# Performance work log

Measured on AMD Instinct MI355X. Metric: run time of the kernel, lower is better.

The kernel has to match this reference:

```python
import jax, jax.numpy as jnp
import numpy as np

NUM_NODES = 50000
NUM_EDGES = 800000
DIM = 96


def setup_inputs() -> dict:
    key = jax.random.key(0)
    k1, k2, k3, k4, k5, k6 = jax.random.split(key, 6)
    x = jax.random.normal(k1, (NUM_NODES, DIM), dtype=jnp.float32)
    edge_index = jax.random.randint(k2, (2, NUM_EDGES), 0, NUM_NODES, dtype=jnp.int64)
    s = 1.0 / np.sqrt(DIM)
    W_self = jax.random.uniform(k3, (DIM, DIM), dtype=jnp.float32, minval=-s, maxval=s)
    b_self = jax.random.uniform(k4, (DIM,), dtype=jnp.float32, minval=-s, maxval=s)
    W_neigh = jax.random.uniform(k5, (DIM, DIM), dtype=jnp.float32, minval=-s, maxval=s)
    b_neigh = jax.random.uniform(k6, (DIM,), dtype=jnp.float32, minval=-s, maxval=s)
    return {"x": x, "edge_index": edge_index, "W_self": W_self, "b_self": b_self,
            "W_neigh": W_neigh, "b_neigh": b_neigh}


def reference(x, edge_index, W_self, b_self, W_neigh, b_neigh):
    source, target = edge_index[0], edge_index[1]
    # scatter-add of gathered source features into target rows
    aggregated = jax.ops.segment_sum(x[source], target, num_segments=NUM_NODES)  # [N, D]
    degree = jax.ops.segment_sum(jnp.ones((NUM_EDGES,), dtype=x.dtype), target,
                                 num_segments=NUM_NODES)[:, None]  # [N, 1]
    neighbor_mean = aggregated / jnp.maximum(degree, 1.0)
    # nn.Linear applies x @ W.T + b
    return x @ W_self.T + b_self + neighbor_mean @ W_neigh.T + b_neigh
```

## Files before the change

### kernel.cpp

```cpp
#include <hip/hip_runtime.h>
#include <hip/hip_bf16.h>

#define N_NODES 50000
#define N_EDGES 800000
#define DIM 96
#define NPART 256
#define PSZ 196
#define NBINBLK 196
#define BINCAP 48
#define BPP (NBINBLK * BINCAP)
#define CAP 4096
#define NPACK_BLOCKS 4688

typedef unsigned int uint;
typedef unsigned short u16;

__device__ __forceinline__ u16 f2bf(float f) {
    __hip_bfloat16 h = __float2bfloat16(f);
    return *reinterpret_cast<u16*>(&h);
}
__device__ __forceinline__ float bf2f(u16 u) {
    return __uint_as_float(((uint)u) << 16);
}
__device__ __forceinline__ int pdiv(int t) { return (int)(((uint)t * 85599u) >> 24); }

__global__ __launch_bounds__(256) void packbin_k(
    const float* __restrict__ x, const int* __restrict__ ei,
    u16* __restrict__ xbf, uint* __restrict__ part_edges,
    int* __restrict__ counts)
{
    __shared__ uint bins[NPART * BINCAP];
    __shared__ int  bcnt[NPART];
    const int tid = threadIdx.x;

    if (blockIdx.x >= NBINBLK) {
        int pb = blockIdx.x - NBINBLK;
        int i4 = (pb * 256 + tid) * 4;
        if (i4 < N_NODES * DIM) {
            float4 v = *reinterpret_cast<const float4*>(x + i4);
            ushort4 o;
            o.x = f2bf(v.x); o.y = f2bf(v.y); o.z = f2bf(v.z); o.w = f2bf(v.w);
            *reinterpret_cast<ushort4*>(xbf + i4) = o;
        }
        return;
    }

    for (int i = tid; i < NPART; i += 256) bcnt[i] = 0;
    __syncthreads();

    const int e0 = blockIdx.x * 4096 + tid * 16;
    if (e0 + 16 <= N_EDGES) {
#pragma unroll
        for (int j = 0; j < 4; j++) {
            int4 s = *reinterpret_cast<const int4*>(ei + e0 + j * 4);
            int4 t = *reinterpret_cast<const int4*>(ei + N_EDGES + e0 + j * 4);
            int ss[4] = {s.x, s.y, s.z, s.w};
            int tt[4] = {t.x, t.y, t.z, t.w};
#pragma unroll
            for (int k = 0; k < 4; k++) {
                int p = pdiv(tt[k]);
                int local = tt[k] - p * PSZ;
                int slot = atomicAdd(&bcnt[p], 1);
                if (slot < BINCAP)
                    bins[p * BINCAP + slot] = ((uint)local << 16) | (uint)ss[k];
            }
        }
    } else {
        for (int j = 0; j < 16; j++) {
            int e = e0 + j;
            if (e < N_EDGES) {
                int sv = ei[e];
                int tv = ei[N_EDGES + e];
                int p = pdiv(tv);
                int local = tv - p * PSZ;
                int slot = atomicAdd(&bcnt[p], 1);
                if (slot < BINCAP)
                    bins[p * BINCAP + slot] = ((uint)local << 16) | (uint)sv;
            }
        }
    }
    __syncthreads();

    for (int p = tid; p < NPART; p += 256)
        counts[p * NBINBLK + blockIdx.x] = min(bcnt[p], BINCAP);

    for (int i = tid; i < NPART * BINCAP; i += 256) {
        int p = i / BINCAP;
        int s = i - p * BINCAP;
        if (s < bcnt[p])
            part_edges[(size_t)p * BPP + blockIdx.x * BINCAP + s] = bins[i];
    }
}

__global__ __launch_bounds__(1024) void fused_k(
    const u16* __restrict__ xbf,
    const uint* __restrict__ part_edges,
    const int* __restrict__ counts,
    const float* __restrict__ Wself, const float* __restrict__ bself,
    const float* __restrict__ Wneigh, const float* __restrict__ bneigh,
    float* __restrict__ out)
{
    using short8 = __attribute__((ext_vector_type(8))) short;
    using f32x4  = __attribute__((ext_vector_type(4))) float;

    __shared__ u16   Axm[208 * 200];
    __shared__ short Bb[96 * 200];
    __shared__ uint  recs[CAP];
    __shared__ u16   ssrc[CAP];
    __shared__ int   bc[256];
    __shared__ int   csc[256];
    __shared__ int   hist[256];
    __shared__ int   cur[256];

    const int tid = threadIdx.x;
    const int p = blockIdx.x;
    const int node0 = p * PSZ;

    for (int idx = tid; idx < 96 * 96; idx += 1024) {
        int j = idx / 96;
        int k = idx - j * 96;
        Bb[j * 200 + k]      = (short)f2bf(Wself[idx]);
        Bb[j * 200 + 96 + k] = (short)f2bf(Wneigh[idx]);
    }

    if (tid < 256) {
        int v = (tid < NBINBLK) ? counts[p * NBINBLK + tid] : 0;
        bc[tid] = v;
        csc[tid] = v;
        cur[tid] = 0;
    }

    for (int i = tid; i < PSZ * 12; i += 1024) {
        int n = i / 12, t = i - n * 12;
        int node = node0 + n;
        short8 v = (short8)0;
        if (node < N_NODES)
            v = *reinterpret_cast<const short8*>(xbf + (size_t)node * DIM + t * 8);
        *reinterpret_cast<short8*>(&Axm[n * 200 + t * 8]) = v;
    }
    __syncthreads();

    for (int o = 1; o < 256; o <<= 1) {
        int v = 0;
        if (tid < 256 && tid >= o) v = csc[tid - o];
        __syncthreads();
        if (tid < 256) csc[tid] += v;
        __syncthreads();
    }
    int m = csc[255]; if (m > CAP) m = CAP;

    for (int i = tid; i < NBINBLK * BINCAP; i += 1024) {
        int b = i / BINCAP;
        int s = i - b * BINCAP;
        if (s < bc[b]) {
            int dst = csc[b] - bc[b] + s;
            if (dst < CAP)
                recs[dst] = part_edges[(size_t)p * BPP + i];
        }
    }
    __syncthreads();

    for (int i = tid; i < m; i += 1024)
        atomicAdd(&cur[recs[i] >> 16], 1);
    __syncthreads();
    if (tid < 256) hist[tid] = cur[tid];
    __syncthreads();
    for (int o = 1; o < 256; o <<= 1) {
        int v = 0;
        if (tid < 256 && tid >= o) v = hist[tid - o];
        __syncthreads();
        if (tid < 256) hist[tid] += v;
        __syncthreads();
    }
    if (tid < 256) cur[tid] = hist[tid] - cur[tid];
    __syncthreads();

    for (int i = tid; i < m; i += 1024) {
        uint r = recs[i];
        int pos = atomicAdd(&cur[r >> 16], 1);
        ssrc[pos] = (u16)(r & 0xFFFF);
    }
    __syncthreads();

    if (tid < 1008) {
        const int g = tid / 24;
        const int l = tid - g * 24;
        const int l4 = l * 4;
        for (int r = g; r < PSZ; r += 42) {
            int end = hist[r];
            int beg = (r > 0) ? hist[r - 1] : 0;
            float ax = 0.f, ay = 0.f, az = 0.f, aw = 0.f;
            int i = beg;
            for (; i + 3 < end; i += 4) {
                int s0 = ssrc[i], s1 = ssrc[i + 1], s2 = ssrc[i + 2], s3 = ssrc[i + 3];
                ushort4 v0 = *reinterpret_cast<const ushort4*>(xbf + (size_t)s0 * DIM + l4);
                ushort4 v1 = *reinterpret_cast<const ushort4*>(xbf + (size_t)s1 * DIM + l4);
                ushort4 v2 = *reinterpret_cast<const ushort4*>(xbf + (size_t)s2 * DIM + l4);
                ushort4 v3 = *reinterpret_cast<const ushort4*>(xbf + (size_t)s3 * DIM + l4);
                ax += bf2f(v0.x) + bf2f(v1.x) + bf2f(v2.x) + bf2f(v3.x);
                ay += bf2f(v0.y) + bf2f(v1.y) + bf2f(v2.y) + bf2f(v3.y);
                az += bf2f(v0.z) + bf2f(v1.z) + bf2f(v2.z) + bf2f(v3.z);
                aw += bf2f(v0.w) + bf2f(v1.w) + bf2f(v2.w) + bf2f(v3.w);
            }
            for (; i < end; i++) {
                int s = ssrc[i];
                ushort4 v = *reinterpret_cast<const ushort4*>(xbf + (size_t)s * DIM + l4);
                ax += bf2f(v.x); ay += bf2f(v.y); az += bf2f(v.z); aw += bf2f(v.w);
            }
            float inv = (end > beg) ? 1.0f / (float)(end - beg) : 0.f;
            ushort4 o;
            o.x = f2bf(ax * inv); o.y = f2bf(ay * inv);
            o.z = f2bf(az * inv); o.w = f2bf(aw * inv);
            *reinterpret_cast<ushort4*>(&Axm[r * 200 + 96 + l4]) = o;
        }
    }
    __syncthreads();

    const int wave = tid >> 6;
    const int lane = tid & 63;
    const int quad = lane >> 4;
    const int m16  = lane & 15;

    if (wave < 13) {
        const int rloc = wave * 16;
        f32x4 acc[6];
#pragma unroll
        for (int nt = 0; nt < 6; nt++) acc[nt] = (f32x4){0.f, 0.f, 0.f, 0.f};

#pragma unroll
        for (int kt = 0; kt < 6; kt++) {
            short8 a = *reinterpret_cast<const short8*>(
                &Axm[(rloc + m16) * 200 + kt * 32 + quad * 8]);
#pragma unroll
            for (int nt = 0; nt < 6; nt++) {
                short8 b = *reinterpret_cast<const short8*>(
                    &Bb[(nt * 16 + m16) * 200 + kt * 32 + quad * 8]);
                acc[nt] = __builtin_amdgcn_mfma_f32_16x16x32_bf16(a, b, acc[nt], 0, 0, 0);
            }
        }

#pragma unroll
        for (int nt = 0; nt < 6; nt++) {
            int col = nt * 16 + m16;
            float bias = bself[col] + bneigh[col];
#pragma unroll
            for (int reg = 0; reg < 4; reg++) {
                int rl = rloc + quad * 4 + reg;
                int row = node0 + rl;
                if (rl < PSZ && row < N_NODES)
                    out[(size_t)row * DIM + col] = acc[nt][reg] + bias;
            }
        }
    }
}

extern "C" void kernel_launch(void* const* d_in, const int* in_sizes, int n_in,
                              void* d_out, int out_size, void* d_ws, size_t ws_size,
                              hipStream_t stream) {
    const float* x      = (const float*)d_in[0];
    const int*   ei     = (const int*)d_in[1];
    const float* Wself  = (const float*)d_in[2];
    const float* bself  = (const float*)d_in[3];
    const float* Wneigh = (const float*)d_in[4];
    const float* bneigh = (const float*)d_in[5];
    float* out = (float*)d_out;

    uint* part_edges = (uint*)d_ws;
    int*  counts     = (int*)(part_edges + (size_t)NPART * BPP);
    u16*  xbf        = (u16*)(counts + NPART * NBINBLK);

    packbin_k<<<NBINBLK + NPACK_BLOCKS, 256, 0, stream>>>(
        x, ei, xbf, part_edges, counts);
    fused_k<<<NPART, 1024, 0, stream>>>(
        xbf, part_edges, counts, Wself, bself, Wneigh, bneigh, out);
}
```

Baseline: 126.8 us.

## Merge binning and fused compute into one cooperative kernel with grid sync

Replaces the two-kernel pipeline (bin/pack kernel then fused aggregate+GEMM kernel) with a single cooperative launch of 256 blocks of 1024 threads. Each block first converts part of x to bf16 and bins its slice of edges into shared memory, then a grid-wide sync separates this from the per-partition aggregation and MFMA phase. It removes one kernel launch boundary and lets the W staging overlap the binning, at the cost of fewer, larger binning blocks (lower parallelism in phase one), grid sync overhead, and a single large shared-memory buffer reused across phases.

```diff
diff --git a/kernel.cpp b/kernel.cpp
--- a/kernel.cpp
+++ b/kernel.cpp
@@ -1,16 +1,18 @@
 #include <hip/hip_runtime.h>
 #include <hip/hip_bf16.h>
+#include <hip/hip_cooperative_groups.h>
 
 #define N_NODES 50000
 #define N_EDGES 800000
 #define DIM 96
 #define NPART 256
 #define PSZ 196
-#define NBINBLK 196
 #define BINCAP 48
-#define BPP (NBINBLK * BINCAP)
+#define BPP (NPART * BINCAP)
 #define CAP 4096
-#define NPACK_BLOCKS 4688
+#define EPB (N_EDGES / NPART)
+
+namespace cg = cooperative_groups;
 
 typedef unsigned int uint;
 typedef unsigned short u16;
@@ -24,97 +26,30 @@
 }
 __device__ __forceinline__ int pdiv(int t) { return (int)(((uint)t * 85599u) >> 24); }
 
-__global__ __launch_bounds__(256) void packbin_k(
+__global__ __launch_bounds__(1024) void sage_all_k(
     const float* __restrict__ x, const int* __restrict__ ei,
-    u16* __restrict__ xbf, uint* __restrict__ part_edges,
-    int* __restrict__ counts)
-{
-    __shared__ uint bins[NPART * BINCAP];
-    __shared__ int  bcnt[NPART];
-    const int tid = threadIdx.x;
-
-    if (blockIdx.x >= NBINBLK) {
-        int pb = blockIdx.x - NBINBLK;
-        int i4 = (pb * 256 + tid) * 4;
-        if (i4 < N_NODES * DIM) {
-            float4 v = *reinterpret_cast<const float4*>(x + i4);
-            ushort4 o;
-            o.x = f2bf(v.x); o.y = f2bf(v.y); o.z = f2bf(v.z); o.w = f2bf(v.w);
-            *reinterpret_cast<ushort4*>(xbf + i4) = o;
-        }
-        return;
-    }
-
-    for (int i = tid; i < NPART; i += 256) bcnt[i] = 0;
-    __syncthreads();
-
-    const int e0 = blockIdx.x * 4096 + tid * 16;
-    if (e0 + 16 <= N_EDGES) {
-#pragma unroll
-        for (int j = 0; j < 4; j++) {
-            int4 s = *reinterpret_cast<const int4*>(ei + e0 + j * 4);
-            int4 t = *reinterpret_cast<const int4*>(ei + N_EDGES + e0 + j * 4);
-            int ss[4] = {s.x, s.y, s.z, s.w};
-            int tt[4] = {t.x, t.y, t.z, t.w};
-#pragma unroll
-            for (int k = 0; k < 4; k++) {
-                int p = pdiv(tt[k]);
-                int local = tt[k] - p * PSZ;
-                int slot = atomicAdd(&bcnt[p], 1);
-                if (slot < BINCAP)
-                    bins[p * BINCAP + slot] = ((uint)local << 16) | (uint)ss[k];
-            }
-        }
-    } else {
-        for (int j = 0; j < 16; j++) {
-            int e = e0 + j;
-            if (e < N_EDGES) {
-                int sv = ei[e];
-                int tv = ei[N_EDGES + e];
-                int p = pdiv(tv);
-                int local = tv - p * PSZ;
-                int slot = atomicAdd(&bcnt[p], 1);
-                if (slot < BINCAP)
-                    bins[p * BINCAP + slot] = ((uint)local << 16) | (uint)sv;
-            }
-        }
-    }
-    __syncthreads();
-
-    for (int p = tid; p < NPART; p += 256)
-        counts[p * NBINBLK + blockIdx.x] = min(bcnt[p], BINCAP);
-
-    for (int i = tid; i < NPART * BINCAP; i += 256) {
-        int p = i / BINCAP;
-        int s = i - p * BINCAP;
-        if (s < bcnt[p])
-            part_edges[(size_t)p * BPP + blockIdx.x * BINCAP + s] = bins[i];
-    }
-}
-
-__global__ __launch_bounds__(1024) void fused_k(
-    const u16* __restrict__ xbf,
-    const uint* __restrict__ part_edges,
-    const int* __restrict__ counts,
     const float* __restrict__ Wself, const float* __restrict__ bself,
     const float* __restrict__ Wneigh, const float* __restrict__ bneigh,
-    float* __restrict__ out)
+    u16* __restrict__ xbf, uint* __restrict__ part_edges,
+    int* __restrict__ counts, float* __restrict__ out)
 {
     using short8 = __attribute__((ext_vector_type(8))) short;
     using f32x4  = __attribute__((ext_vector_type(4))) float;
 
-    __shared__ u16   Axm[208 * 200];
-    __shared__ short Bb[96 * 200];
-    __shared__ uint  recs[CAP];
-    __shared__ u16   ssrc[CAP];
-    __shared__ int   bc[256];
-    __shared__ int   csc[256];
-    __shared__ int   hist[256];
-    __shared__ int   cur[256];
+    __shared__ __align__(16) char smem[150272];
+    u16*   Axm  = (u16*)smem;
+    short* Bb   = (short*)(smem + 83200);
+    uint*  recs = (uint*)(smem + 121600);
+    u16*   ssrc = (u16*)(smem + 137984);
+    int*   bc   = (int*)(smem + 146176);
+    int*   csc  = (int*)(smem + 147200);
+    int*   hist = (int*)(smem + 148224);
+    int*   cur  = (int*)(smem + 149248);
+    uint*  bins = (uint*)smem;
+    int*   bcnt = (int*)(smem + 49152);
 
     const int tid = threadIdx.x;
-    const int p = blockIdx.x;
-    const int node0 = p * PSZ;
+    const int b = blockIdx.x;
 
     for (int idx = tid; idx < 96 * 96; idx += 1024) {
         int j = idx / 96;
@@ -123,8 +58,41 @@
         Bb[j * 200 + 96 + k] = (short)f2bf(Wneigh[idx]);
     }
 
+    for (int i = b * 1024 + tid; i < N_NODES * DIM / 4; i += NPART * 1024) {
+        float4 v = reinterpret_cast<const float4*>(x)[i];
+        ushort4 o;
+        o.x = f2bf(v.x); o.y = f2bf(v.y); o.z = f2bf(v.z); o.w = f2bf(v.w);
+        reinterpret_cast<ushort4*>(xbf)[i] = o;
+    }
+
+    if (tid < NPART) bcnt[tid] = 0;
+    __syncthreads();
+    for (int i = tid; i < EPB; i += 1024) {
+        int e = b * EPB + i;
+        int sv = ei[e];
+        int tv = ei[N_EDGES + e];
+        int p = pdiv(tv);
+        int local = tv - p * PSZ;
+        int slot = atomicAdd(&bcnt[p], 1);
+        if (slot < BINCAP)
+            bins[p * BINCAP + slot] = ((uint)local << 16) | (uint)sv;
+    }
+    __syncthreads();
+    if (tid < NPART) counts[tid * NPART + b] = min(bcnt[tid], BINCAP);
+    for (int i = tid; i < NPART * BINCAP; i += 1024) {
+        int p = i / BINCAP;
+        int s = i - p * BINCAP;
+        if (s < bcnt[p])
+            part_edges[(size_t)p * BPP + b * BINCAP + s] = bins[i];
+    }
+
+    cg::this_grid().sync();
+
+    const int p = b;
+    const int node0 = p * PSZ;
+
     if (tid < 256) {
-        int v = (tid < NBINBLK) ? counts[p * NBINBLK + tid] : 0;
+        int v = counts[p * NPART + tid];
         bc[tid] = v;
         csc[tid] = v;
         cur[tid] = 0;
@@ -149,11 +117,11 @@
     }
     int m = csc[255]; if (m > CAP) m = CAP;
 
-    for (int i = tid; i < NBINBLK * BINCAP; i += 1024) {
-        int b = i / BINCAP;
-        int s = i - b * BINCAP;
-        if (s < bc[b]) {
-            int dst = csc[b] - bc[b] + s;
+    for (int i = tid; i < NPART * BINCAP; i += 1024) {
+        int cb = i / BINCAP;
+        int s = i - cb * BINCAP;
+        if (s < bc[cb]) {
+            int dst = csc[cb] - bc[cb] + s;
             if (dst < CAP)
                 recs[dst] = part_edges[(size_t)p * BPP + i];
         }
@@ -233,9 +201,9 @@
                 &Axm[(rloc + m16) * 200 + kt * 32 + quad * 8]);
 #pragma unroll
             for (int nt = 0; nt < 6; nt++) {
-                short8 b = *reinterpret_cast<const short8*>(
+                short8 bb = *reinterpret_cast<const short8*>(
                     &Bb[(nt * 16 + m16) * 200 + kt * 32 + quad * 8]);
-                acc[nt] = __builtin_amdgcn_mfma_f32_16x16x32_bf16(a, b, acc[nt], 0, 0, 0);
+                acc[nt] = __builtin_amdgcn_mfma_f32_16x16x32_bf16(a, bb, acc[nt], 0, 0, 0);
             }
         }
 
@@ -267,10 +235,13 @@
 
     uint* part_edges = (uint*)d_ws;
     int*  counts     = (int*)(part_edges + (size_t)NPART * BPP);
-    u16*  xbf        = (u16*)(counts + NPART * NBINBLK);
-
-    packbin_k<<<NBINBLK + NPACK_BLOCKS, 256, 0, stream>>>(
-        x, ei, xbf, part_edges, counts);
-    fused_k<<<NPART, 1024, 0, stream>>>(
-        xbf, part_edges, counts, Wself, bself, Wneigh, bneigh, out);
-}
+    u16*  xbf        = (u16*)(counts + NPART * NPART);
+
+    void* args[] = {
+        (void*)&x, (void*)&ei, (void*)&Wself, (void*)&bself,
+        (void*)&Wneigh, (void*)&bneigh,
+        (void*)&xbf, (void*)&part_edges, (void*)&counts, (void*)&out
+    };
+    hipLaunchCooperativeKernel((void*)sage_all_k, dim3(NPART), dim3(1024),
+                               args, 0, stream);
+}
```

Result: slower. 165.1 us (+30.2%).
